# Performance work log

Measured on AMD Instinct MI355X. Metric: run time of the kernel, lower is better.

## Reference

```python
import jax, jax.numpy as jnp
import numpy as np

D, H, W, C = 24, 24, 16, 2        # image_dims + num_classes
THETA_ALPHA = 160.0               # bilateral spatial std
THETA_BETA = 3.0                  # bilateral intensity std
THETA_GAMMA = 3.0                 # spatial-only std
NUM_ITERATIONS = 5
N = D * H * W


def _gauss_kernel(feats):
    # Dense Gaussian kernel K_ij = exp(-0.5 * ||f_i - f_j||^2).
    # This is the exact filter that the permutohedral lattice approximates
    # (self-term included, matching the lattice splat/blur/slice behaviour).
    sq = jnp.sum(feats * feats, axis=-1)               # [N]
    d2 = sq[:, None] + sq[None, :] - 2.0 * feats @ feats.T
    return jnp.exp(-0.5 * jnp.maximum(d2, 0.0))        # [N, N]


def _positions():
    zz, yy, xx = jnp.meshgrid(jnp.arange(D), jnp.arange(H), jnp.arange(W), indexing='ij')
    return jnp.stack([zz, yy, xx], axis=-1).reshape(N, 3).astype(jnp.float32)


def setup_inputs() -> dict:
    key = jax.random.key(0)
    k1, k2 = jax.random.split(key)
    unaries = jax.random.normal(k1, (1, D, H, W, C), dtype=jnp.float32)
    rgb = jax.random.uniform(k2, (1, D, H, W, 1), dtype=jnp.float32)
    # learned params (build() initial values)
    spatial_ker_weights = jnp.array([1.41, 1.41], dtype=jnp.float32)
    bilateral_ker_weights = jnp.array([3.85, 3.85], dtype=jnp.float32)
    compatibility_matrix = jnp.eye(C, dtype=jnp.float32)
    return dict(unaries=unaries, rgb=rgb,
                spatial_ker_weights=spatial_ker_weights,
                bilateral_ker_weights=bilateral_ker_weights,
                compatibility_matrix=compatibility_matrix)


def reference(unaries, rgb, spatial_ker_weights, bilateral_ker_weights, compatibility_matrix):
    out_shape = unaries.shape
    u = unaries.reshape(N, C)                 # batch index 0 only, as in the TF code
    img = rgb.reshape(N, -1)
    pos = _positions()

    Ks = _gauss_kernel(pos / THETA_GAMMA)                                        # spatial kernel [N,N]
    Kb = _gauss_kernel(jnp.concatenate([pos / THETA_ALPHA, img / THETA_BETA], -1))  # bilateral kernel [N,N]

    # normalization = filter applied to all-ones (row sums)
    norm_s = jnp.sum(Ks, axis=-1, keepdims=True)   # [N,1]
    norm_b = jnp.sum(Kb, axis=-1, keepdims=True)   # [N,1]

    q = u
    for _ in range(NUM_ITERATIONS):
        spatial_out = (Ks @ q) / norm_s            # [N,C]
        bilateral_out = (Kb @ q) / norm_b          # [N,C]
        # diag(w_s) @ spatial.T + diag(w_b) @ bilateral.T  ==  per-class scaling
        message = spatial_out * spatial_ker_weights + bilateral_out * bilateral_ker_weights
        pairwise = message @ compatibility_matrix.T  # (compat @ msg.T).T
        q = u - pairwise
    return q.reshape(out_shape)
```

## Files before the change

kernel.cpp:

```cpp
#include <hip/hip_runtime.h>


#define DD 24
#define HH 24
#define WW 16
#define SLICE 384
#define NPTS 9216
#define NT 5
#define TP 12
#define LPITCH 196
#define LOG2E 1.4426950408889634f
#define K3L   (LOG2E / 18.0f)
#define K160L (LOG2E / 51200.0f)

static __device__ __forceinline__ int iabs(int a) { return a < 0 ? -a : a; }

static __device__ __forceinline__ void xy_conv12(
        float* sA, float* sB, const float* g3, const float* g160,
        int y, int x, const float v[12], float ov[12]) {
    float4* wrow = (float4*)(sA + y * LPITCH + x * 12);
    wrow[0] = make_float4(v[0], v[1], v[2], v[3]);
    wrow[1] = make_float4(v[4], v[5], v[6], v[7]);
    wrow[2] = make_float4(v[8], v[9], v[10], v[11]);
    __syncthreads();

    float ax[12];
#pragma unroll
    for (int f = 0; f < 12; ++f) ax[f] = 0.f;
    const float4* rowy = (const float4*)(sA + y * LPITCH);
#pragma unroll
    for (int xp = 0; xp < WW; ++xp) {
        int d = iabs(x - xp);
        float w3 = g3[d], wb = g160[d];
        float4 a0 = rowy[xp * 3 + 0];
        float4 a1 = rowy[xp * 3 + 1];
        float4 a2 = rowy[xp * 3 + 2];
        ax[0] = fmaf(w3, a0.x, ax[0]);  ax[1] = fmaf(w3, a0.y, ax[1]);
        ax[2] = fmaf(wb, a0.z, ax[2]);  ax[3] = fmaf(wb, a0.w, ax[3]);
        ax[4] = fmaf(wb, a1.x, ax[4]);  ax[5] = fmaf(wb, a1.y, ax[5]);
        ax[6] = fmaf(wb, a1.z, ax[6]);  ax[7] = fmaf(wb, a1.w, ax[7]);
        ax[8] = fmaf(wb, a2.x, ax[8]);  ax[9] = fmaf(wb, a2.y, ax[9]);
        ax[10] = fmaf(wb, a2.z, ax[10]); ax[11] = fmaf(wb, a2.w, ax[11]);
    }
    __syncthreads();
    float4* wrowB = (float4*)(sB + y * LPITCH + x * 12);
    wrowB[0] = make_float4(ax[0], ax[1], ax[2], ax[3]);
    wrowB[1] = make_float4(ax[4], ax[5], ax[6], ax[7]);
    wrowB[2] = make_float4(ax[8], ax[9], ax[10], ax[11]);
    __syncthreads();

#pragma unroll
    for (int f = 0; f < 12; ++f) ov[f] = 0.f;
#pragma unroll
    for (int yp = 0; yp < HH; ++yp) {
        int d = iabs(y - yp);
        float w3 = g3[d], wb = g160[d];
        const float4* col = (const float4*)(sB + yp * LPITCH + x * 12);
        float4 b0 = col[0];
        float4 b1 = col[1];
        float4 b2 = col[2];
        ov[0] = fmaf(w3, b0.x, ov[0]);  ov[1] = fmaf(w3, b0.y, ov[1]);
        ov[2] = fmaf(wb, b0.z, ov[2]);  ov[3] = fmaf(wb, b0.w, ov[3]);
        ov[4] = fmaf(wb, b1.x, ov[4]);  ov[5] = fmaf(wb, b1.y, ov[5]);
        ov[6] = fmaf(wb, b1.z, ov[6]);  ov[7] = fmaf(wb, b1.w, ov[7]);
        ov[8] = fmaf(wb, b2.x, ov[8]);  ov[9] = fmaf(wb, b2.y, ov[9]);
        ov[10] = fmaf(wb, b2.z, ov[10]); ov[11] = fmaf(wb, b2.w, ov[11]);
    }
    __syncthreads();
}

static __device__ __forceinline__ void write12(float* dst, const float ov[12]) {
    float4* pd = (float4*)dst;
    pd[0] = make_float4(ov[0], ov[1], ov[2], ov[3]);
    pd[1] = make_float4(ov[4], ov[5], ov[6], ov[7]);
    pd[2] = make_float4(ov[8], ov[9], ov[10], ov[11]);
}

__global__ __launch_bounds__(SLICE)
void crf_pre(const float2* __restrict__ u2, const float* __restrict__ rgb,
             float* __restrict__ tmpA, float* __restrict__ tmpN) {
    __shared__ float g3[32];
    __shared__ float g160[32];
    __shared__ float sA[HH * LPITCH];
    __shared__ float sB[HH * LPITCH];
    const int z = blockIdx.x;
    const int t = threadIdx.x;
    const int y = t >> 4, x = t & 15;
    const int i = z * SLICE + t;

    if (t < DD) {
        g3[t] = exp2f(-(float)(t * t) * K3L);
        g160[t] = exp2f(-(float)(t * t) * K160L);
    }
    __syncthreads();

    const float I3 = rgb[i] * (1.0f / 3.0f);
    const float E = exp2f(-0.5f * LOG2E * I3 * I3);
    float Pt[NT];
    Pt[0] = E;
#pragma unroll
    for (int k = 1; k < NT; ++k) Pt[k] = Pt[k - 1] * I3;
    const float2 uu = u2[i];

    float v[12], ov[12];
#pragma unroll
    for (int f = 0; f < 12; ++f) v[f] = 0.f;
#pragma unroll
    for (int k = 0; k < NT; ++k) v[2 + k] = Pt[k];
    xy_conv12(sA, sB, g3, g160, y, x, v, ov);
    write12(tmpN + (size_t)i * TP, ov);

    v[0] = uu.x; v[1] = uu.y;
#pragma unroll
    for (int k = 0; k < NT; ++k) { v[2 + 2 * k] = Pt[k] * uu.x; v[3 + 2 * k] = Pt[k] * uu.y; }
    xy_conv12(sA, sB, g3, g160, y, x, v, ov);
    write12(tmpA + (size_t)i * TP, ov);
}

__global__ __launch_bounds__(SLICE)
void crf_iter(const float* __restrict__ tsrc, float* __restrict__ tdst,
              const float* __restrict__ tmpN, float* __restrict__ normb,
              const float* __restrict__ rgb, const float2* __restrict__ u2,
              const float* __restrict__ sw, const float* __restrict__ bw,
              const float* __restrict__ compat,
              float2* __restrict__ out, int it) {
    __shared__ float g3[32];
    __shared__ float g160[32];
    __shared__ float sA[HH * LPITCH];
    __shared__ float sB[HH * LPITCH];
    const int z = blockIdx.x;
    const int t = threadIdx.x;
    const int y = t >> 4, x = t & 15;
    const int i = z * SLICE + t;

    if (t < DD) {
        g3[t] = exp2f(-(float)(t * t) * K3L);
        g160[t] = exp2f(-(float)(t * t) * K160L);
    }
    __syncthreads();

    float acc[12];
#pragma unroll
    for (int f = 0; f < 12; ++f) acc[f] = 0.f;
    {
        const float* p = tsrc + (size_t)t * TP;
#pragma unroll 4
        for (int zp = 0; zp < DD; ++zp) {
            int d = iabs(z - zp);
            float w3 = g3[d], wb = g160[d];
            float4 a0 = ((const float4*)p)[0];
            float4 a1 = ((const float4*)p)[1];
            float4 a2 = ((const float4*)p)[2];
            acc[0] = fmaf(w3, a0.x, acc[0]);  acc[1] = fmaf(w3, a0.y, acc[1]);
            acc[2] = fmaf(wb, a0.z, acc[2]);  acc[3] = fmaf(wb, a0.w, acc[3]);
            acc[4] = fmaf(wb, a1.x, acc[4]);  acc[5] = fmaf(wb, a1.y, acc[5]);
            acc[6] = fmaf(wb, a1.z, acc[6]);  acc[7] = fmaf(wb, a1.w, acc[7]);
            acc[8] = fmaf(wb, a2.x, acc[8]);  acc[9] = fmaf(wb, a2.y, acc[9]);
            acc[10] = fmaf(wb, a2.z, acc[10]); acc[11] = fmaf(wb, a2.w, acc[11]);
            p += (size_t)SLICE * TP;
        }
    }

    const float I3 = rgb[i] * (1.0f / 3.0f);
    const float E = exp2f(-0.5f * LOG2E * I3 * I3);
    const float invf[NT] = {1.f, 1.f, 0.5f, 1.f / 6.f, 1.f / 24.f};
    float Pt[NT];
    Pt[0] = E;
#pragma unroll
    for (int k = 1; k < NT; ++k) Pt[k] = Pt[k - 1] * I3;

    float inv_nb;
    if (it == 0) {
        float accN[NT] = {0.f, 0.f, 0.f, 0.f, 0.f};
        const float* pn = tmpN + (size_t)t * TP;
#pragma unroll 4
        for (int zp = 0; zp < DD; ++zp) {
            float wb = g160[iabs(z - zp)];
            float4 n0 = ((const float4*)pn)[0];
            float4 n1 = ((const float4*)pn)[1];
            accN[0] = fmaf(wb, n0.z, accN[0]);
            accN[1] = fmaf(wb, n0.w, accN[1]);
            accN[2] = fmaf(wb, n1.x, accN[2]);
            accN[3] = fmaf(wb, n1.y, accN[3]);
            accN[4] = fmaf(wb, n1.z, accN[4]);
            pn += (size_t)SLICE * TP;
        }
        float nb = 0.f;
#pragma unroll
        for (int k = 0; k < NT; ++k) nb = fmaf(Pt[k] * invf[k], accN[k], nb);
        normb[i] = nb;
        inv_nb = 1.0f / nb;
    } else {
        inv_nb = 1.0f / normb[i];
    }

    float sx = 0.f, sy = 0.f, sz = 0.f;
#pragma unroll
    for (int xp = 0; xp < WW; ++xp) sx += g3[iabs(x - xp)];
#pragma unroll
    for (int yp = 0; yp < HH; ++yp) sy += g3[iabs(y - yp)];
#pragma unroll
    for (int zp = 0; zp < DD; ++zp) sz += g3[iabs(z - zp)];
    const float inv_ns = 1.0f / (sx * sy * sz);

    float s0 = acc[0] * inv_ns;
    float s1 = acc[1] * inv_ns;
    float b0 = 0.f, b1 = 0.f;
#pragma unroll
    for (int k = 0; k < NT; ++k) {
        float w = Pt[k] * invf[k];
        b0 = fmaf(w, acc[2 + 2 * k], b0);
        b1 = fmaf(w, acc[3 + 2 * k], b1);
    }
    b0 *= inv_nb;
    b1 *= inv_nb;
    float m0 = s0 * sw[0] + b0 * bw[0];
    float m1 = s1 * sw[1] + b1 * bw[1];
    float p0 = fmaf(compat[0], m0, compat[1] * m1);
    float p1 = fmaf(compat[2], m0, compat[3] * m1);
    const float2 uu = u2[i];
    float q0 = uu.x - p0;
    float q1 = uu.y - p1;

    if (it == 4) {
        out[i] = make_float2(q0, q1);
        return;
    }

    float v[12], ov[12];
    v[0] = q0; v[1] = q1;
#pragma unroll
    for (int k = 0; k < NT; ++k) { v[2 + 2 * k] = Pt[k] * q0; v[3 + 2 * k] = Pt[k] * q1; }
    xy_conv12(sA, sB, g3, g160, y, x, v, ov);
    write12(tdst + (size_t)i * TP, ov);
}

extern "C" void kernel_launch(void* const* d_in, const int* in_sizes, int n_in,
                              void* d_out, int out_size, void* d_ws, size_t ws_size,
                              hipStream_t stream) {
    const float2* u2     = (const float2*)d_in[0];
    const float*  rgb    = (const float*)d_in[1];
    const float*  sw     = (const float*)d_in[2];
    const float*  bw     = (const float*)d_in[3];
    const float*  compat = (const float*)d_in[4];
    float2* out = (float2*)d_out;

    float* ws = (float*)d_ws;
    float* tmpA  = ws;
    float* tmpB  = ws + NPTS * TP;
    float* tmpN  = ws + 2 * NPTS * TP;
    float* normb = ws + 3 * NPTS * TP;

    crf_pre<<<DD, SLICE, 0, stream>>>(u2, rgb, tmpA, tmpN);

    const float* tsrc = tmpA;
    float* tdst = tmpB;
    for (int it = 0; it < 5; ++it) {
        crf_iter<<<DD, SLICE, 0, stream>>>(tsrc, tdst, tmpN, normb, rgb, u2,
                                           sw, bw, compat, out, it);
        const float* ns = tdst;
        tdst = (float*)tsrc;
        tsrc = ns;
    }
}
```

Baseline: 120.4 us.

## Replace bilateral xy convolution with low-order spatial moment expansion per slice

The wide-sigma (160) bilateral spatial Gaussian in x and y is replaced by a second-order Taylor expansion around the slice centre, so each z-slice only needs 9 polynomial moments per feature instead of a full separable xy convolution over 10 channels. The xy convolution now carries only the 2 spatial-kernel channels, and the per-iteration global traffic drops from 12 floats per voxel to 2 floats per voxel plus small moment tables. Bilateral normalisation is recomputed each iteration from the moments instead of being cached. The trade-off is extra approximation error from truncating the Gaussian expansion, plus the shuffle reductions and serial moment accumulation done by a few threads.

```diff
diff --git a/kernel.cpp b/kernel.cpp
--- a/kernel.cpp
+++ b/kernel.cpp
@@ -7,213 +7,233 @@
 #define SLICE 384
 #define NPTS 9216
 #define NT 5
-#define TP 12
-#define LPITCH 196
+#define NF 10
+#define MSTRIDE 96
+#define NSTRIDE 48
 #define LOG2E 1.4426950408889634f
 #define K3L   (LOG2E / 18.0f)
 #define K160L (LOG2E / 51200.0f)
+#define UU    (1.0f / 51200.0f)
 
 static __device__ __forceinline__ int iabs(int a) { return a < 0 ? -a : a; }
 
-static __device__ __forceinline__ void xy_conv12(
-        float* sA, float* sB, const float* g3, const float* g160,
-        int y, int x, const float v[12], float ov[12]) {
-    float4* wrow = (float4*)(sA + y * LPITCH + x * 12);
-    wrow[0] = make_float4(v[0], v[1], v[2], v[3]);
-    wrow[1] = make_float4(v[4], v[5], v[6], v[7]);
-    wrow[2] = make_float4(v[8], v[9], v[10], v[11]);
-    __syncthreads();
-
-    float ax[12];
-#pragma unroll
-    for (int f = 0; f < 12; ++f) ax[f] = 0.f;
-    const float4* rowy = (const float4*)(sA + y * LPITCH);
+static __device__ __forceinline__ float rowred16(float v) {
+    v += __shfl_xor(v, 1, 16);
+    v += __shfl_xor(v, 2, 16);
+    v += __shfl_xor(v, 4, 16);
+    v += __shfl_xor(v, 8, 16);
+    return v;
+}
+
+template <int NFF>
+static __device__ void slice_moments(const float* f, const float* xpw,
+                                     int y, int x, int t,
+                                     float (*rowsum)[52], float* gdst) {
+    for (int F = 0; F < NFF; ++F) {
+#pragma unroll
+        for (int a = 0; a < 5; ++a) {
+            float r = rowred16(f[F] * xpw[a]);
+            if (x == 0) rowsum[y][F * 5 + a] = r;
+        }
+    }
+    __syncthreads();
+    if (t < NFF) {
+        float acc[9];
+#pragma unroll
+        for (int k = 0; k < 9; ++k) acc[k] = 0.f;
+        for (int yy = 0; yy < HH; ++yy) {
+            float yc = (float)yy - 11.5f;
+            float yc2 = yc * yc, yc3 = yc2 * yc, yc4 = yc2 * yc2;
+            const float* S = rowsum[yy] + t * 5;
+            float S0 = S[0], S1 = S[1], S2 = S[2], S3 = S[3], S4 = S[4];
+            acc[0] += S0;
+            acc[1] += S1;
+            acc[2] += yc * S0;
+            acc[3] += S2;
+            acc[4] += yc * S1;
+            acc[5] += yc2 * S0;
+            acc[6] += S3 + yc2 * S1;
+            acc[7] += yc * S2 + yc3 * S0;
+            acc[8] += S4 + 2.f * yc2 * S2 + yc4 * S0;
+        }
+#pragma unroll
+        for (int k = 0; k < 9; ++k) gdst[t * 9 + k] = acc[k];
+    }
+    __syncthreads();
+}
+
+static __device__ void xyconv2(float2 q, int y, int x, const float* g3s,
+                               float2 (*cA)[17], float2 (*cB)[17], float2* ov) {
+    cA[y][x] = q;
+    __syncthreads();
+    float a0 = 0.f, a1 = 0.f;
 #pragma unroll
     for (int xp = 0; xp < WW; ++xp) {
-        int d = iabs(x - xp);
-        float w3 = g3[d], wb = g160[d];
-        float4 a0 = rowy[xp * 3 + 0];
-        float4 a1 = rowy[xp * 3 + 1];
-        float4 a2 = rowy[xp * 3 + 2];
-        ax[0] = fmaf(w3, a0.x, ax[0]);  ax[1] = fmaf(w3, a0.y, ax[1]);
-        ax[2] = fmaf(wb, a0.z, ax[2]);  ax[3] = fmaf(wb, a0.w, ax[3]);
-        ax[4] = fmaf(wb, a1.x, ax[4]);  ax[5] = fmaf(wb, a1.y, ax[5]);
-        ax[6] = fmaf(wb, a1.z, ax[6]);  ax[7] = fmaf(wb, a1.w, ax[7]);
-        ax[8] = fmaf(wb, a2.x, ax[8]);  ax[9] = fmaf(wb, a2.y, ax[9]);
-        ax[10] = fmaf(wb, a2.z, ax[10]); ax[11] = fmaf(wb, a2.w, ax[11]);
-    }
-    __syncthreads();
-    float4* wrowB = (float4*)(sB + y * LPITCH + x * 12);
-    wrowB[0] = make_float4(ax[0], ax[1], ax[2], ax[3]);
-    wrowB[1] = make_float4(ax[4], ax[5], ax[6], ax[7]);
-    wrowB[2] = make_float4(ax[8], ax[9], ax[10], ax[11]);
-    __syncthreads();
-
-#pragma unroll
-    for (int f = 0; f < 12; ++f) ov[f] = 0.f;
+        float w = g3s[iabs(x - xp)];
+        float2 v = cA[y][xp];
+        a0 = fmaf(w, v.x, a0);
+        a1 = fmaf(w, v.y, a1);
+    }
+    cB[y][x] = make_float2(a0, a1);
+    __syncthreads();
+    float b0 = 0.f, b1 = 0.f;
 #pragma unroll
     for (int yp = 0; yp < HH; ++yp) {
-        int d = iabs(y - yp);
-        float w3 = g3[d], wb = g160[d];
-        const float4* col = (const float4*)(sB + yp * LPITCH + x * 12);
-        float4 b0 = col[0];
-        float4 b1 = col[1];
-        float4 b2 = col[2];
-        ov[0] = fmaf(w3, b0.x, ov[0]);  ov[1] = fmaf(w3, b0.y, ov[1]);
-        ov[2] = fmaf(wb, b0.z, ov[2]);  ov[3] = fmaf(wb, b0.w, ov[3]);
-        ov[4] = fmaf(wb, b1.x, ov[4]);  ov[5] = fmaf(wb, b1.y, ov[5]);
-        ov[6] = fmaf(wb, b1.z, ov[6]);  ov[7] = fmaf(wb, b1.w, ov[7]);
-        ov[8] = fmaf(wb, b2.x, ov[8]);  ov[9] = fmaf(wb, b2.y, ov[9]);
-        ov[10] = fmaf(wb, b2.z, ov[10]); ov[11] = fmaf(wb, b2.w, ov[11]);
-    }
-    __syncthreads();
-}
-
-static __device__ __forceinline__ void write12(float* dst, const float ov[12]) {
-    float4* pd = (float4*)dst;
-    pd[0] = make_float4(ov[0], ov[1], ov[2], ov[3]);
-    pd[1] = make_float4(ov[4], ov[5], ov[6], ov[7]);
-    pd[2] = make_float4(ov[8], ov[9], ov[10], ov[11]);
+        float w = g3s[iabs(y - yp)];
+        float2 v = cB[yp][x];
+        b0 = fmaf(w, v.x, b0);
+        b1 = fmaf(w, v.y, b1);
+    }
+    *ov = make_float2(b0, b1);
+    __syncthreads();
 }
 
 __global__ __launch_bounds__(SLICE)
 void crf_pre(const float2* __restrict__ u2, const float* __restrict__ rgb,
-             float* __restrict__ tmpA, float* __restrict__ tmpN) {
-    __shared__ float g3[32];
-    __shared__ float g160[32];
-    __shared__ float sA[HH * LPITCH];
-    __shared__ float sB[HH * LPITCH];
-    const int z = blockIdx.x;
-    const int t = threadIdx.x;
+             float2* __restrict__ tmpS, float* __restrict__ tmpM,
+             float* __restrict__ tmpMN) {
+    __shared__ float g3s[32];
+    __shared__ float2 cA[HH][17];
+    __shared__ float2 cB[HH][17];
+    __shared__ float rowsum[HH][52];
+
+    const int z = blockIdx.x, t = threadIdx.x;
     const int y = t >> 4, x = t & 15;
     const int i = z * SLICE + t;
 
-    if (t < DD) {
-        g3[t] = exp2f(-(float)(t * t) * K3L);
-        g160[t] = exp2f(-(float)(t * t) * K160L);
-    }
-    __syncthreads();
-
-    const float I3 = rgb[i] * (1.0f / 3.0f);
+    if (t < DD) g3s[t] = exp2f(-(float)(t * t) * K3L);
+    __syncthreads();
+
+    const float I3 = rgb[i] * (1.f / 3.f);
     const float E = exp2f(-0.5f * LOG2E * I3 * I3);
     float Pt[NT];
     Pt[0] = E;
 #pragma unroll
     for (int k = 1; k < NT; ++k) Pt[k] = Pt[k - 1] * I3;
-    const float2 uu = u2[i];
-
-    float v[12], ov[12];
-#pragma unroll
-    for (int f = 0; f < 12; ++f) v[f] = 0.f;
-#pragma unroll
-    for (int k = 0; k < NT; ++k) v[2 + k] = Pt[k];
-    xy_conv12(sA, sB, g3, g160, y, x, v, ov);
-    write12(tmpN + (size_t)i * TP, ov);
-
-    v[0] = uu.x; v[1] = uu.y;
-#pragma unroll
-    for (int k = 0; k < NT; ++k) { v[2 + 2 * k] = Pt[k] * uu.x; v[3 + 2 * k] = Pt[k] * uu.y; }
-    xy_conv12(sA, sB, g3, g160, y, x, v, ov);
-    write12(tmpA + (size_t)i * TP, ov);
+    const float2 qq = u2[i];
+
+    float2 sxy;
+    xyconv2(qq, y, x, g3s, cA, cB, &sxy);
+    tmpS[i] = sxy;
+
+    const float xc = (float)x - 7.5f;
+    float xpw[5] = {1.f, xc, xc * xc, xc * xc * xc, xc * xc * xc * xc};
+
+    float f[NF];
+#pragma unroll
+    for (int k = 0; k < NT; ++k) { f[2 * k] = Pt[k] * qq.x; f[2 * k + 1] = Pt[k] * qq.y; }
+    slice_moments<NF>(f, xpw, y, x, t, rowsum, tmpM + z * MSTRIDE);
+
+    float fN[NT];
+#pragma unroll
+    for (int k = 0; k < NT; ++k) fN[k] = Pt[k];
+    slice_moments<NT>(fN, xpw, y, x, t, rowsum, tmpMN + z * NSTRIDE);
 }
 
 __global__ __launch_bounds__(SLICE)
-void crf_iter(const float* __restrict__ tsrc, float* __restrict__ tdst,
-              const float* __restrict__ tmpN, float* __restrict__ normb,
+void crf_iter(const float2* __restrict__ tmpS_src, const float* __restrict__ tmpM_src,
+              const float* __restrict__ tmpMN,
+              float2* __restrict__ tmpS_dst, float* __restrict__ tmpM_dst,
               const float* __restrict__ rgb, const float2* __restrict__ u2,
               const float* __restrict__ sw, const float* __restrict__ bw,
               const float* __restrict__ compat,
               float2* __restrict__ out, int it) {
-    __shared__ float g3[32];
-    __shared__ float g160[32];
-    __shared__ float sA[HH * LPITCH];
-    __shared__ float sB[HH * LPITCH];
-    const int z = blockIdx.x;
-    const int t = threadIdx.x;
+    __shared__ float g3s[32];
+    __shared__ float g160zs[32];
+    __shared__ float2 cA[HH][17];
+    __shared__ float2 cB[HH][17];
+    __shared__ float rowsum[HH][52];
+    __shared__ float MbS[90];
+    __shared__ float MbNS[45];
+
+    const int z = blockIdx.x, t = threadIdx.x;
     const int y = t >> 4, x = t & 15;
     const int i = z * SLICE + t;
 
     if (t < DD) {
-        g3[t] = exp2f(-(float)(t * t) * K3L);
-        g160[t] = exp2f(-(float)(t * t) * K160L);
-    }
-    __syncthreads();
-
-    float acc[12];
-#pragma unroll
-    for (int f = 0; f < 12; ++f) acc[f] = 0.f;
-    {
-        const float* p = tsrc + (size_t)t * TP;
-#pragma unroll 4
-        for (int zp = 0; zp < DD; ++zp) {
-            int d = iabs(z - zp);
-            float w3 = g3[d], wb = g160[d];
-            float4 a0 = ((const float4*)p)[0];
-            float4 a1 = ((const float4*)p)[1];
-            float4 a2 = ((const float4*)p)[2];
-            acc[0] = fmaf(w3, a0.x, acc[0]);  acc[1] = fmaf(w3, a0.y, acc[1]);
-            acc[2] = fmaf(wb, a0.z, acc[2]);  acc[3] = fmaf(wb, a0.w, acc[3]);
-            acc[4] = fmaf(wb, a1.x, acc[4]);  acc[5] = fmaf(wb, a1.y, acc[5]);
-            acc[6] = fmaf(wb, a1.z, acc[6]);  acc[7] = fmaf(wb, a1.w, acc[7]);
-            acc[8] = fmaf(wb, a2.x, acc[8]);  acc[9] = fmaf(wb, a2.y, acc[9]);
-            acc[10] = fmaf(wb, a2.z, acc[10]); acc[11] = fmaf(wb, a2.w, acc[11]);
-            p += (size_t)SLICE * TP;
-        }
-    }
-
-    const float I3 = rgb[i] * (1.0f / 3.0f);
+        g3s[t] = exp2f(-(float)(t * t) * K3L);
+        g160zs[t] = exp2f(-(float)(t * t) * K160L);
+    }
+    __syncthreads();
+
+    float zs0 = 0.f, zs1 = 0.f;
+    for (int zp = 0; zp < DD; ++zp) {
+        float w = g3s[iabs(z - zp)];
+        float2 v = tmpS_src[zp * SLICE + t];
+        zs0 = fmaf(w, v.x, zs0);
+        zs1 = fmaf(w, v.y, zs1);
+    }
+
+    if (t < 90) {
+        float acc = 0.f;
+        for (int zp = 0; zp < DD; ++zp)
+            acc = fmaf(g160zs[iabs(z - zp)], tmpM_src[zp * MSTRIDE + t], acc);
+        MbS[t] = acc;
+    } else if (t >= 128 && t < 173) {
+        int m = t - 128;
+        float acc = 0.f;
+        for (int zp = 0; zp < DD; ++zp)
+            acc = fmaf(g160zs[iabs(z - zp)], tmpMN[zp * NSTRIDE + m], acc);
+        MbNS[m] = acc;
+    }
+    __syncthreads();
+
+    const float xc = (float)x - 7.5f, yc = (float)y - 11.5f;
+    const float Ri = xc * xc + yc * yc;
+    const float uq = UU * UU;
+    const float omuR = 1.f - UU * Ri;
+    float CF[9];
+    CF[0] = 1.f - UU * Ri + 0.5f * uq * Ri * Ri;
+    CF[1] = 2.f * UU * xc * omuR;
+    CF[2] = 2.f * UU * yc * omuR;
+    CF[3] = (-UU + uq * Ri) + 2.f * uq * xc * xc;
+    CF[4] = 4.f * uq * xc * yc;
+    CF[5] = (-UU + uq * Ri) + 2.f * uq * yc * yc;
+    CF[6] = -2.f * uq * xc;
+    CF[7] = -2.f * uq * yc;
+    CF[8] = 0.5f * uq;
+
+    const float I3 = rgb[i] * (1.f / 3.f);
     const float E = exp2f(-0.5f * LOG2E * I3 * I3);
-    const float invf[NT] = {1.f, 1.f, 0.5f, 1.f / 6.f, 1.f / 24.f};
     float Pt[NT];
     Pt[0] = E;
 #pragma unroll
     for (int k = 1; k < NT; ++k) Pt[k] = Pt[k - 1] * I3;
-
-    float inv_nb;
-    if (it == 0) {
-        float accN[NT] = {0.f, 0.f, 0.f, 0.f, 0.f};
-        const float* pn = tmpN + (size_t)t * TP;
-#pragma unroll 4
-        for (int zp = 0; zp < DD; ++zp) {
-            float wb = g160[iabs(z - zp)];
-            float4 n0 = ((const float4*)pn)[0];
-            float4 n1 = ((const float4*)pn)[1];
-            accN[0] = fmaf(wb, n0.z, accN[0]);
-            accN[1] = fmaf(wb, n0.w, accN[1]);
-            accN[2] = fmaf(wb, n1.x, accN[2]);
-            accN[3] = fmaf(wb, n1.y, accN[3]);
-            accN[4] = fmaf(wb, n1.z, accN[4]);
-            pn += (size_t)SLICE * TP;
-        }
-        float nb = 0.f;
-#pragma unroll
-        for (int k = 0; k < NT; ++k) nb = fmaf(Pt[k] * invf[k], accN[k], nb);
-        normb[i] = nb;
-        inv_nb = 1.0f / nb;
-    } else {
-        inv_nb = 1.0f / normb[i];
-    }
-
-    float sx = 0.f, sy = 0.f, sz = 0.f;
-#pragma unroll
-    for (int xp = 0; xp < WW; ++xp) sx += g3[iabs(x - xp)];
-#pragma unroll
-    for (int yp = 0; yp < HH; ++yp) sy += g3[iabs(y - yp)];
-#pragma unroll
-    for (int zp = 0; zp < DD; ++zp) sz += g3[iabs(z - zp)];
-    const float inv_ns = 1.0f / (sx * sy * sz);
-
-    float s0 = acc[0] * inv_ns;
-    float s1 = acc[1] * inv_ns;
-    float b0 = 0.f, b1 = 0.f;
+    const float invf[NT] = {1.f, 1.f, 0.5f, 1.f / 6.f, 1.f / 24.f};
+
+    float sxn = 0.f, syn = 0.f, szn = 0.f;
+#pragma unroll
+    for (int xp = 0; xp < WW; ++xp) sxn += g3s[iabs(x - xp)];
+#pragma unroll
+    for (int yp = 0; yp < HH; ++yp) syn += g3s[iabs(y - yp)];
+#pragma unroll
+    for (int zp = 0; zp < DD; ++zp) szn += g3s[iabs(z - zp)];
+    const float inv_ns = 1.0f / (sxn * syn * szn);
+
+    float nb = 0.f, b0 = 0.f, b1 = 0.f;
 #pragma unroll
     for (int k = 0; k < NT; ++k) {
         float w = Pt[k] * invf[k];
-        b0 = fmaf(w, acc[2 + 2 * k], b0);
-        b1 = fmaf(w, acc[3 + 2 * k], b1);
-    }
+        float sN = 0.f, s0 = 0.f, s1 = 0.f;
+        const float* MN = MbNS + k * 9;
+        const float* M0 = MbS + (2 * k) * 9;
+        const float* M1 = MbS + (2 * k + 1) * 9;
+#pragma unroll
+        for (int m = 0; m < 9; ++m) {
+            sN = fmaf(CF[m], MN[m], sN);
+            s0 = fmaf(CF[m], M0[m], s0);
+            s1 = fmaf(CF[m], M1[m], s1);
+        }
+        nb = fmaf(w, sN, nb);
+        b0 = fmaf(w, s0, b0);
+        b1 = fmaf(w, s1, b1);
+    }
+    float inv_nb = 1.0f / nb;
     b0 *= inv_nb;
     b1 *= inv_nb;
+
+    float s0 = zs0 * inv_ns;
+    float s1 = zs1 * inv_ns;
     float m0 = s0 * sw[0] + b0 * bw[0];
     float m1 = s1 * sw[1] + b1 * bw[1];
     float p0 = fmaf(compat[0], m0, compat[1] * m1);
@@ -227,12 +247,15 @@
         return;
     }
 
-    float v[12], ov[12];
-    v[0] = q0; v[1] = q1;
-#pragma unroll
-    for (int k = 0; k < NT; ++k) { v[2 + 2 * k] = Pt[k] * q0; v[3 + 2 * k] = Pt[k] * q1; }
-    xy_conv12(sA, sB, g3, g160, y, x, v, ov);
-    write12(tdst + (size_t)i * TP, ov);
+    float2 sxy;
+    xyconv2(make_float2(q0, q1), y, x, g3s, cA, cB, &sxy);
+    tmpS_dst[i] = sxy;
+
+    float xpw[5] = {1.f, xc, xc * xc, xc * xc * xc, xc * xc * xc * xc};
+    float f[NF];
+#pragma unroll
+    for (int k = 0; k < NT; ++k) { f[2 * k] = Pt[k] * q0; f[2 * k + 1] = Pt[k] * q1; }
+    slice_moments<NF>(f, xpw, y, x, t, rowsum, tmpM_dst + z * MSTRIDE);
 }
 
 extern "C" void kernel_launch(void* const* d_in, const int* in_sizes, int n_in,
@@ -246,20 +269,20 @@
     float2* out = (float2*)d_out;
 
     float* ws = (float*)d_ws;
-    float* tmpA  = ws;
-    float* tmpB  = ws + NPTS * TP;
-    float* tmpN  = ws + 2 * NPTS * TP;
-    float* normb = ws + 3 * NPTS * TP;
-
-    crf_pre<<<DD, SLICE, 0, stream>>>(u2, rgb, tmpA, tmpN);
-
-    const float* tsrc = tmpA;
-    float* tdst = tmpB;
+    float2* tmpS_A = (float2*)ws;
+    float2* tmpS_B = (float2*)(ws + 2 * NPTS);
+    float*  tmpM_A = ws + 4 * NPTS;
+    float*  tmpM_B = tmpM_A + DD * MSTRIDE;
+    float*  tmpMN  = tmpM_B + DD * MSTRIDE;
+
+    crf_pre<<<DD, SLICE, 0, stream>>>(u2, rgb, tmpS_A, tmpM_A, tmpMN);
+
+    const float2* sS = tmpS_A; float2* dS = tmpS_B;
+    const float*  sM = tmpM_A; float*  dM = tmpM_B;
     for (int it = 0; it < 5; ++it) {
-        crf_iter<<<DD, SLICE, 0, stream>>>(tsrc, tdst, tmpN, normb, rgb, u2,
-                                           sw, bw, compat, out, it);
-        const float* ns = tdst;
-        tdst = (float*)tsrc;
-        tsrc = ns;
-    }
-}
+        crf_iter<<<DD, SLICE, 0, stream>>>(sS, sM, tmpMN, dS, dM,
+                                           rgb, u2, sw, bw, compat, out, it);
+        const float2* nS = dS; dS = (float2*)sS; sS = nS;
+        const float*  nM = dM; dM = (float*)sM; sM = nM;
+    }
+}
```

Result: slower. 135.3 us (+12.4%).
